# Kernel tuning notes

Measured on AMD Instinct MI355X. Metric: run time of the kernel, lower is better.

The kernel has to match this reference:

```python
import jax, jax.numpy as jnp
import numpy as np

B, Nq, C = 1, 40000, 256
Hh, L, P = 8, 4, 8
hd = C // Hh
LEVEL_SHAPES = [(128, 128), (64, 64), (32, 32), (16, 16)]


def setup_inputs() -> dict:
    key = jax.random.key(0)
    ks = jax.random.split(key, 16)
    inp = {}
    inp['query'] = jax.random.normal(ks[0], (B, Nq, C), jnp.float32)
    # reference points in [-1, 1] normalized coords (x, y)
    inp['reference_points'] = jax.random.uniform(ks[1], (B, Nq, L, 2), jnp.float32) * 2.0 - 1.0
    for i, (h, w) in enumerate(LEVEL_SHAPES):
        inp[f'feat{i}'] = jax.random.normal(ks[2 + i], (B, C, h, w), jnp.float32)
    # learned params (torch Linear y = x @ W + b, W stored as [in, out])
    inp['W_off'] = jax.random.normal(ks[6], (C, Hh * L * P * 2), jnp.float32) * 0.02
    inp['b_off'] = jax.random.normal(ks[7], (Hh * L * P * 2,), jnp.float32) * 0.5
    inp['W_attn'] = jax.random.normal(ks[8], (C, Hh * L * P), jnp.float32) * 0.02
    inp['b_attn'] = jnp.zeros((Hh * L * P,), jnp.float32)
    inp['W_val'] = jax.random.normal(ks[9], (C, C), jnp.float32) * (1.0 / np.sqrt(C))
    inp['b_val'] = jnp.zeros((C,), jnp.float32)
    inp['W_out'] = jax.random.normal(ks[10], (C, C), jnp.float32) * (1.0 / np.sqrt(C))
    inp['b_out'] = jnp.zeros((C,), jnp.float32)
    return inp


def _deform_sample(v, coords):
    # Bilinear grid_sample, align_corners=True, zeros padding.
    # v: [B, Hh, H, W, hd]; coords: [B, Hh, S, 2] in [-1, 1] (x, y)
    _, _, H, W, _ = v.shape
    x = (coords[..., 0] + 1.0) * 0.5 * (W - 1)
    y = (coords[..., 1] + 1.0) * 0.5 * (H - 1)
    x0 = jnp.floor(x)
    y0 = jnp.floor(y)
    vflat = v.reshape(v.shape[0], v.shape[1], H * W, v.shape[4])

    def corner(xi, yi, w):
        inb = (xi >= 0) & (xi <= W - 1) & (yi >= 0) & (yi <= H - 1)
        idx = (jnp.clip(yi, 0, H - 1) * W + jnp.clip(xi, 0, W - 1)).astype(jnp.int32)
        g = jnp.take_along_axis(vflat, idx[..., None], axis=2)  # [B,Hh,S,hd]
        return g * (w * inb)[..., None]

    return (corner(x0, y0, (x0 + 1 - x) * (y0 + 1 - y))
            + corner(x0 + 1, y0, (x - x0) * (y0 + 1 - y))
            + corner(x0, y0 + 1, (x0 + 1 - x) * (y - y0))
            + corner(x0 + 1, y0 + 1, (x - x0) * (y - y0)))


def reference(query, feat0, feat1, feat2, feat3, reference_points,
              W_off, b_off, W_attn, b_attn, W_val, b_val, W_out, b_out):
    feats = [feat0, feat1, feat2, feat3]
    off = (query @ W_off + b_off).reshape(B, Nq, Hh, L, P, 2)
    w = (query @ W_attn + b_attn).reshape(B, Nq, Hh, L, P)
    w = jax.nn.softmax(w, axis=-1)  # softmax over points, per level
    # samp: [B, Nq, Hh, L, P, 2]
    samp = reference_points[:, :, None, :, None, :] + jnp.tanh(off) * 0.25

    out = jnp.zeros((B, Nq, Hh, hd), jnp.float32)
    for l, f in enumerate(feats):
        Hl, Wl = f.shape[2], f.shape[3]
        v = jnp.einsum('bchw,cd->bhwd', f, W_val) + b_val  # value proj
        v = v.reshape(B, Hl, Wl, Hh, hd).transpose(0, 3, 1, 2, 4)  # [B,Hh,H,W,hd]
        coords = samp[:, :, :, l].transpose(0, 2, 1, 3, 4).reshape(B, Hh, Nq * P, 2)
        s = _deform_sample(v, coords).reshape(B, Hh, Nq, P, hd)
        wl = w[:, :, :, l].transpose(0, 2, 1, 3)  # [B,Hh,Nq,P]
        out = out + jnp.einsum('bhnpd,bhnp->bnhd', s, wl)

    return out.reshape(B, Nq, C) @ W_out + b_out
```

## Files before the change

### kernel.cpp

```cpp
#include <hip/hip_runtime.h>
#include <hip/hip_fp16.h>
#include <math.h>

#define NQ 40000

typedef short s16x8 __attribute__((ext_vector_type(8)));
typedef float f32x4 __attribute__((ext_vector_type(4)));

static constexpr int HLa[4] = {128, 64, 32, 16};
static constexpr int HWa[4] = {16384, 4096, 1024, 256};
static constexpr int VB[4] = {0, 4194304, 5242880, 5505024};

__device__ __forceinline__ short bf16hi(float x) {
    union { float f; unsigned u; } v; v.f = x;
    unsigned r = v.u + 0x7FFFu + ((v.u >> 16) & 1u);
    return (short)(r >> 16);
}
__device__ __forceinline__ float bf16f(short s) {
    union { unsigned u; float f; } v; v.u = ((unsigned)(unsigned short)s) << 16;
    return v.f;
}
__device__ __forceinline__ float fast_tanh(float x) {
    float xc = fminf(fmaxf(x, -15.f), 15.f);
    float e = __expf(2.f * xc);
    return (e - 1.f) / (e + 1.f);
}
#define MFMA16(a, b, c) __builtin_amdgcn_mfma_f32_16x16x32_bf16(a, b, c, 0, 0, 0)

__global__ __launch_bounds__(256) void prep_w(
    const float* __restrict__ Woff, const float* __restrict__ Wattn,
    const float* __restrict__ Wout, short* __restrict__ WtH, short* __restrict__ WtL)
{
    int r = blockIdx.x, c = threadIdx.x;
    float x;
    if (r < 512)      x = Woff[c * 512 + r];
    else if (r < 768) x = Wattn[c * 256 + (r - 512)];
    else              x = Wout[c * 256 + (r - 768)];
    short hi = bf16hi(x);
    WtH[r * 256 + c] = hi;
    WtL[r * 256 + c] = bf16hi(x - bf16f(hi));
}

__global__ __launch_bounds__(256) void vproj_kernel(
    const float* __restrict__ f0, const float* __restrict__ f1,
    const float* __restrict__ f2, const float* __restrict__ f3,
    const float* __restrict__ Wv, const float* __restrict__ bv,
    __half* __restrict__ v)
{
    __shared__ float fT[256 * 16];

    int bid = blockIdx.x;
    const float* f;
    int base, HWl, hw0;
    if (bid < 1024)      { f = f0; base = VB[0]; HWl = 16384; hw0 = bid * 16; }
    else if (bid < 1280) { f = f1; base = VB[1]; HWl = 4096;  hw0 = (bid - 1024) * 16; }
    else if (bid < 1344) { f = f2; base = VB[2]; HWl = 1024;  hw0 = (bid - 1280) * 16; }
    else                 { f = f3; base = VB[3]; HWl = 256;   hw0 = (bid - 1344) * 16; }

    int t = threadIdx.x;
    for (int k = 0; k < 16; ++k) {
        int idx = k * 256 + t;
        int c = idx >> 4, j = idx & 15;
        fT[idx] = f[c * HWl + hw0 + j];
    }
    __syncthreads();

    int to4 = (t & 63) * 4;
    int hw4 = (t >> 6) * 4;

    float4 bv4 = *(const float4*)(bv + to4);
    float acc[4][4];
    #pragma unroll
    for (int i = 0; i < 4; ++i) {
        acc[i][0] = bv4.x; acc[i][1] = bv4.y; acc[i][2] = bv4.z; acc[i][3] = bv4.w;
    }

    #pragma unroll 4
    for (int c = 0; c < 256; ++c) {
        float4 w4 = *(const float4*)(Wv + c * 256 + to4);
        float4 fv = *(const float4*)(fT + c * 16 + hw4);
        float fa[4] = {fv.x, fv.y, fv.z, fv.w};
        float wa[4] = {w4.x, w4.y, w4.z, w4.w};
        #pragma unroll
        for (int i = 0; i < 4; ++i)
            #pragma unroll
            for (int j = 0; j < 4; ++j)
                acc[i][j] += fa[i] * wa[j];
    }

    int hh = to4 >> 5, dd4 = to4 & 31;
    #pragma unroll
    for (int i = 0; i < 4; ++i) {
        int hw = hw0 + hw4 + i;
        __half2 h0 = __floats2half2_rn(acc[i][0], acc[i][1]);
        __half2 h1 = __floats2half2_rn(acc[i][2], acc[i][3]);
        uint2 st = make_uint2(*(unsigned*)&h0, *(unsigned*)&h1);
        *(uint2*)(v + base + (hh * HWl + hw) * 32 + dd4) = st;
    }
}

__global__ __launch_bounds__(256, 4) void msda_kernel(
    const float* __restrict__ query, const float* __restrict__ refp,
    const float* __restrict__ boff,  const float* __restrict__ battn,
    const float* __restrict__ bout,
    const short* __restrict__ WtH,   const short* __restrict__ WtL,
    const __half* __restrict__ v,    float* __restrict__ out)
{
    __shared__ __align__(16) char lds[28928];
    short*    sQh  = (short*)lds;
    short*    sQl  = (short*)(lds + 8448);
    __half*   sWh  = (__half*)(lds + 16896);
    float*    sR   = (float*)(lds + 28416);

    const int t = threadIdx.x;
    const int n0 = blockIdx.x * 16;
    const int wv = t >> 6, lane = t & 63;
    const int mrow = lane & 15, kg = lane >> 4;
    float*    offW = (float*)lds + wv * 1056;
    unsigned* sPIw = (unsigned*)(lds + 25344 + wv * 768);
    uint2*    sPWw = (uint2*)(lds + 25344 + wv * 768 + 256);
    __half*   preT = sWh;

    for (int k2 = 0; k2 < 16; ++k2) {
        float x = query[(n0 + k2) * 256 + t];
        short hi = bf16hi(x);
        sQh[k2 * 264 + t] = hi;
        sQl[k2 * 264 + t] = bf16hi(x - bf16f(hi));
    }
    if (t < 128) sR[t] = refp[n0 * 8 + t];
    __syncthreads();

    f32x4 accO[8], accA[4];
    {
        f32x4 z = {0.f, 0.f, 0.f, 0.f};
        #pragma unroll
        for (int j = 0; j < 8; ++j) accO[j] = z;
        #pragma unroll
        for (int j = 0; j < 4; ++j) accA[j] = z;
    }
    {
        const short* offH = WtH + (wv * 128 + mrow) * 256 + kg * 8;
        const short* offLo = WtL + (wv * 128 + mrow) * 256 + kg * 8;
        const short* attH = WtH + (512 + wv * 64 + mrow) * 256 + kg * 8;
        const short* attL = WtL + (512 + wv * 64 + mrow) * 256 + kg * 8;
        const int aoff = mrow * 264 + kg * 8;
        #pragma unroll
        for (int kk = 0; kk < 8; ++kk) {
            s16x8 ah = *(const s16x8*)(sQh + aoff + kk * 32);
            s16x8 al = *(const s16x8*)(sQl + aoff + kk * 32);
            #pragma unroll
            for (int j = 0; j < 8; ++j) {
                s16x8 bh = *(const s16x8*)(offH + j * 4096 + kk * 32);
                s16x8 bl = *(const s16x8*)(offLo + j * 4096 + kk * 32);
                accO[j] = MFMA16(ah, bh, accO[j]);
                accO[j] = MFMA16(al, bh, accO[j]);
                accO[j] = MFMA16(ah, bl, accO[j]);
            }
            #pragma unroll
            for (int ja = 0; ja < 4; ++ja) {
                s16x8 bh = *(const s16x8*)(attH + ja * 4096 + kk * 32);
                s16x8 bl = *(const s16x8*)(attL + ja * 4096 + kk * 32);
                accA[ja] = MFMA16(ah, bh, accA[ja]);
                accA[ja] = MFMA16(al, bh, accA[ja]);
                accA[ja] = MFMA16(ah, bl, accA[ja]);
            }
        }
    }
    #pragma unroll
    for (int j = 0; j < 8; ++j) {
        float bb = boff[wv * 128 + j * 16 + mrow];
        #pragma unroll
        for (int r = 0; r < 4; ++r) accO[j][r] += bb;
    }
    #pragma unroll
    for (int ja = 0; ja < 4; ++ja) {
        float bb = battn[wv * 64 + ja * 16 + mrow];
        #pragma unroll
        for (int r = 0; r < 4; ++r) accA[ja][r] += bb;
    }

    #pragma unroll
    for (int ja = 0; ja < 4; ++ja) {
        int hh = 2 * wv + (ja >> 1);
        int l  = ((ja & 1) << 1) | (mrow >> 3);
        int p  = mrow & 7;
        #pragma unroll
        for (int r = 0; r < 4; ++r) {
            float x = accA[ja][r];
            float m = fmaxf(x, __shfl_xor(x, 1));
            m = fmaxf(m, __shfl_xor(m, 2));
            m = fmaxf(m, __shfl_xor(m, 4));
            float e = __expf(x - m);
            float s = e + __shfl_xor(e, 1);
            s += __shfl_xor(s, 2);
            s += __shfl_xor(s, 4);
            int q = kg * 4 + r;
            sWh[q * 264 + hh * 32 + l * 8 + p] = __float2half_rn(e / s);
        }
    }
    __syncthreads();

    const int l_p = (lane >> 3) & 3, p_p = lane & 7, hhL_p = lane >> 5;
    const int Wl_p = 128 >> l_p;
    const float scl_p = 0.5f * (float)(Wl_p - 1);
    const int whCol = (2 * wv + hhL_p) * 32 + l_p * 8 + p_p;
    const int sg = kg, ch2 = mrow;
    const int Wl_s = 128 >> sg;
    const int HWs = Wl_s * Wl_s;
    const int dyoMul = Wl_s * 16;
    const int VBs = (sg == 0) ? VB[0] : (sg == 1) ? VB[1] : (sg == 2) ? VB[2] : VB[3];
    const __half2* vl0 = (const __half2*)(v + VBs + (2 * wv) * HWs * 32) + ch2;
    const __half2* vl1 = (const __half2*)(v + VBs + (2 * wv + 1) * HWs * 32) + ch2;

    for (int sp = 0; sp < 2; ++sp) {
        if ((kg >> 1) == sp) {
            #pragma unroll
            for (int j = 0; j < 8; ++j)
                #pragma unroll
                for (int r = 0; r < 4; ++r)
                    offW[((kg & 1) * 4 + r) * 132 + j * 16 + mrow] = accO[j][r];
        }

        for (int c8 = 0; c8 < 8; ++c8) {
            const int chunk = sp * 8 + c8;
            {
                float2 ll = *(const float2*)(offW + c8 * 132 + 2 * lane);
                float lx = ll.x, ly = ll.y;
                float w  = __half2float(sWh[chunk * 264 + whCol]);
                float rx = sR[chunk * 8 + l_p * 2], ry = sR[chunk * 8 + l_p * 2 + 1];
                float cx = rx + fast_tanh(lx) * 0.25f;
                float cy = ry + fast_tanh(ly) * 0.25f;
                float xx = (cx + 1.f) * scl_p, yy = (cy + 1.f) * scl_p;
                float x0f = floorf(xx), y0f = floorf(yy);
                float fx = xx - x0f, fy = yy - y0f;
                int x0 = (int)x0f, y0 = (int)y0f;
                int xc0 = min(max(x0, 0), Wl_p - 1);
                int xc1 = min(max(x0 + 1, 0), Wl_p - 1);
                int yc0 = min(max(y0, 0), Wl_p - 1);
                int yc1 = min(max(y0 + 1, 0), Wl_p - 1);
                bool bx0 = (x0 >= 0) & (x0 < Wl_p);
                bool bx1 = (x0 + 1 >= 0) & (x0 + 1 < Wl_p);
                bool by0 = (y0 >= 0) & (y0 < Wl_p);
                bool by1 = (y0 + 1 >= 0) & (y0 + 1 < Wl_p);
                float w00 = (bx0 && by0) ? (1.f - fx) * (1.f - fy) * w : 0.f;
                float w01 = (bx1 && by0) ? fx * (1.f - fy) * w : 0.f;
                float w10 = (bx0 && by1) ? (1.f - fx) * fy * w : 0.f;
                float w11 = (bx1 && by1) ? fx * fy * w : 0.f;
                unsigned pw = (unsigned)(yc0 * Wl_p + xc0)
                            | ((unsigned)(xc1 - xc0) << 14)
                            | ((unsigned)(yc1 - yc0) << 15);
                sPIw[lane] = pw;
                __half2 hA = __floats2half2_rn(w00, w01);
                __half2 hB = __floats2half2_rn(w10, w11);
                sPWw[lane] = make_uint2(*(unsigned*)&hA, *(unsigned*)&hB);
            }

            float ax = 0.f, ay = 0.f;
            #pragma unroll
            for (int iter = 0; iter < 16; ++iter) {
                const int hhL = iter >> 3, p = iter & 7;
                const int rec = hhL * 32 + sg * 8 + p;
                unsigned pw = sPIw[rec];
                uint2 ww = sPWw[rec];
                const __half2* vl = hhL ? vl1 : vl0;
                int idx = pw & 0x3FFF;
                int dxo = ((pw >> 14) & 1) * 16;
                int dyo = ((pw >> 15) & 1) * dyoMul;
                const __half2* b00 = vl + idx * 16;
                float2 fa = __half22float2(*(__half2*)&ww.x);
                float2 fb = __half22float2(*(__half2*)&ww.y);
                float2 f00 = __half22float2(b00[0]);
                float2 f01 = __half22float2(b00[dxo]);
                float2 f10 = __half22float2(b00[dyo]);
                float2 f11 = __half22float2(b00[dxo + dyo]);
                ax += fa.x * f00.x + fa.y * f01.x + fb.x * f10.x + fb.y * f11.x;
                ay += fa.x * f00.y + fa.y * f01.y + fb.x * f10.y + fb.y * f11.y;
                if ((iter & 7) == 7) {
                    float sxv = ax + __shfl_xor(ax, 16); sxv += __shfl_xor(sxv, 32);
                    float syv = ay + __shfl_xor(ay, 16); syv += __shfl_xor(syv, 32);
                    if (sg == 0)
                        *(__half2*)(preT + chunk * 264 + (2 * wv + hhL) * 32 + ch2 * 2) =
                            __floats2half2_rn(sxv, syv);
                    ax = 0.f; ay = 0.f;
                }
            }
        }
    }
    __syncthreads();

    {
        int q = t & 15, seg = t >> 4;
        const __half2* src = (const __half2*)(preT + q * 264 + seg * 16);
        short* dh = sQh + q * 264 + seg * 16;
        short* dl = sQl + q * 264 + seg * 16;
        #pragma unroll
        for (int jj = 0; jj < 8; ++jj) {
            float2 f = __half22float2(src[jj]);
            short h0 = bf16hi(f.x), h1 = bf16hi(f.y);
            dh[2 * jj]     = h0;
            dh[2 * jj + 1] = h1;
            dl[2 * jj]     = bf16hi(f.x - bf16f(h0));
            dl[2 * jj + 1] = bf16hi(f.y - bf16f(h1));
        }
    }
    __syncthreads();

    {
        f32x4 accE[4];
        f32x4 z = {0.f, 0.f, 0.f, 0.f};
        #pragma unroll
        for (int e = 0; e < 4; ++e) accE[e] = z;
        const short* outH = WtH + (768 + wv * 64 + mrow) * 256 + kg * 8;
        const short* outL = WtL + (768 + wv * 64 + mrow) * 256 + kg * 8;
        const int aoff = mrow * 264 + kg * 8;
        #pragma unroll
        for (int kk = 0; kk < 8; ++kk) {
            s16x8 ah = *(const s16x8*)(sQh + aoff + kk * 32);
            s16x8 al = *(const s16x8*)(sQl + aoff + kk * 32);
            #pragma unroll
            for (int e = 0; e < 4; ++e) {
                s16x8 bh = *(const s16x8*)(outH + e * 4096 + kk * 32);
                s16x8 bl = *(const s16x8*)(outL + e * 4096 + kk * 32);
                accE[e] = MFMA16(ah, bh, accE[e]);
                accE[e] = MFMA16(al, bh, accE[e]);
                accE[e] = MFMA16(ah, bl, accE[e]);
            }
        }
        #pragma unroll
        for (int e = 0; e < 4; ++e) {
            int col = wv * 64 + e * 16 + mrow;
            float bb = bout[col];
            #pragma unroll
            for (int r = 0; r < 4; ++r)
                out[(n0 + kg * 4 + r) * 256 + col] = accE[e][r] + bb;
        }
    }
}

extern "C" void kernel_launch(void* const* d_in, const int* in_sizes, int n_in,
                              void* d_out, int out_size, void* d_ws, size_t ws_size,
                              hipStream_t stream) {
    const float* query = (const float*)d_in[0];
    const float* refp  = (const float*)d_in[1];
    const float* f0    = (const float*)d_in[2];
    const float* f1    = (const float*)d_in[3];
    const float* f2    = (const float*)d_in[4];
    const float* f3    = (const float*)d_in[5];
    const float* Woff  = (const float*)d_in[6];
    const float* boff  = (const float*)d_in[7];
    const float* Wattn = (const float*)d_in[8];
    const float* battn = (const float*)d_in[9];
    const float* Wval  = (const float*)d_in[10];
    const float* bval  = (const float*)d_in[11];
    const float* Wout  = (const float*)d_in[12];
    const float* bout  = (const float*)d_in[13];

    __half* v  = (__half*)d_ws;
    short* WtH = (short*)((char*)d_ws + 11141120);
    short* WtL = WtH + 262144;
    float* outp = (float*)d_out;

    prep_w<<<1024, 256, 0, stream>>>(Woff, Wattn, Wout, WtH, WtL);
    vproj_kernel<<<1360, 256, 0, stream>>>(f0, f1, f2, f3, Wval, bval, v);
    msda_kernel<<<2500, 256, 0, stream>>>(query, refp, boff, battn, bout,
                                          WtH, WtL, v, outp);
}
```

Before: 498.7 us.

## Double-buffer sampling records and overlap next-chunk packing with gathers

Splits the per-wave sampling-record buffers into two LDS slots and computes the next chunk's coordinates and bilinear weights while the current chunk's value gathers are in flight. The gather loop is also restructured to issue all four corner loads for four points before consuming them, which exposes more memory-level parallelism. The cost is more LDS per block and higher register pressure from the batched loads, which could reduce occupancy under the 256x4 launch bound.

```diff
diff --git a/kernel.cpp b/kernel.cpp
--- a/kernel.cpp
+++ b/kernel.cpp
@@ -99,6 +99,38 @@
     }
 }
 
+#define PACK_REC(CHUNK, DPI, DPW) do {                                        \
+    float2 ll = *(const float2*)(offW + ((CHUNK) & 7) * 132 + 2 * lane);      \
+    float lx = ll.x, ly = ll.y;                                               \
+    float w  = __half2float(sWh[(CHUNK) * 264 + whCol]);                      \
+    float rx = sR[(CHUNK) * 8 + l_p * 2], ry = sR[(CHUNK) * 8 + l_p * 2 + 1]; \
+    float cx = rx + fast_tanh(lx) * 0.25f;                                    \
+    float cy = ry + fast_tanh(ly) * 0.25f;                                    \
+    float xx = (cx + 1.f) * scl_p, yy = (cy + 1.f) * scl_p;                   \
+    float x0f = floorf(xx), y0f = floorf(yy);                                 \
+    float fx = xx - x0f, fy = yy - y0f;                                       \
+    int x0 = (int)x0f, y0 = (int)y0f;                                         \
+    int xc0 = min(max(x0, 0), Wl_p - 1);                                      \
+    int xc1 = min(max(x0 + 1, 0), Wl_p - 1);                                  \
+    int yc0 = min(max(y0, 0), Wl_p - 1);                                      \
+    int yc1 = min(max(y0 + 1, 0), Wl_p - 1);                                  \
+    bool bx0 = (x0 >= 0) & (x0 < Wl_p);                                       \
+    bool bx1 = (x0 + 1 >= 0) & (x0 + 1 < Wl_p);                               \
+    bool by0 = (y0 >= 0) & (y0 < Wl_p);                                       \
+    bool by1 = (y0 + 1 >= 0) & (y0 + 1 < Wl_p);                               \
+    float w00 = (bx0 && by0) ? (1.f - fx) * (1.f - fy) * w : 0.f;             \
+    float w01 = (bx1 && by0) ? fx * (1.f - fy) * w : 0.f;                     \
+    float w10 = (bx0 && by1) ? (1.f - fx) * fy * w : 0.f;                     \
+    float w11 = (bx1 && by1) ? fx * fy * w : 0.f;                             \
+    unsigned pw = (unsigned)(yc0 * Wl_p + xc0)                                \
+                | ((unsigned)(xc1 - xc0) << 14)                               \
+                | ((unsigned)(yc1 - yc0) << 15);                              \
+    (DPI)[lane] = pw;                                                         \
+    __half2 hA = __floats2half2_rn(w00, w01);                                 \
+    __half2 hB = __floats2half2_rn(w10, w11);                                 \
+    (DPW)[lane] = make_uint2(*(unsigned*)&hA, *(unsigned*)&hB);               \
+} while (0)
+
 __global__ __launch_bounds__(256, 4) void msda_kernel(
     const float* __restrict__ query, const float* __restrict__ refp,
     const float* __restrict__ boff,  const float* __restrict__ battn,
@@ -106,19 +138,21 @@
     const short* __restrict__ WtH,   const short* __restrict__ WtL,
     const __half* __restrict__ v,    float* __restrict__ out)
 {
-    __shared__ __align__(16) char lds[28928];
+    __shared__ __align__(16) char lds[32000];
     short*    sQh  = (short*)lds;
     short*    sQl  = (short*)(lds + 8448);
     __half*   sWh  = (__half*)(lds + 16896);
-    float*    sR   = (float*)(lds + 28416);
+    float*    sR   = (float*)(lds + 31488);
 
     const int t = threadIdx.x;
     const int n0 = blockIdx.x * 16;
     const int wv = t >> 6, lane = t & 63;
     const int mrow = lane & 15, kg = lane >> 4;
     float*    offW = (float*)lds + wv * 1056;
-    unsigned* sPIw = (unsigned*)(lds + 25344 + wv * 768);
-    uint2*    sPWw = (uint2*)(lds + 25344 + wv * 768 + 256);
+    unsigned* sPI0 = (unsigned*)(lds + 25344 + wv * 768);
+    uint2*    sPW0 = (uint2*)(lds + 25344 + wv * 768 + 256);
+    unsigned* sPI1 = (unsigned*)(lds + 28416 + wv * 768);
+    uint2*    sPW1 = (uint2*)(lds + 28416 + wv * 768 + 256);
     __half*   preT = sWh;
 
     for (int k2 = 0; k2 < 16; ++k2) {
@@ -204,6 +238,7 @@
     const int Wl_p = 128 >> l_p;
     const float scl_p = 0.5f * (float)(Wl_p - 1);
     const int whCol = (2 * wv + hhL_p) * 32 + l_p * 8 + p_p;
+    (void)p_p;
     const int sg = kg, ch2 = mrow;
     const int Wl_s = 128 >> sg;
     const int HWs = Wl_s * Wl_s;
@@ -220,69 +255,61 @@
                 for (int r = 0; r < 4; ++r)
                     offW[((kg & 1) * 4 + r) * 132 + j * 16 + mrow] = accO[j][r];
         }
-
+        PACK_REC(sp * 8, sPI0, sPW0);
+
+        #pragma unroll 2
         for (int c8 = 0; c8 < 8; ++c8) {
             const int chunk = sp * 8 + c8;
-            {
-                float2 ll = *(const float2*)(offW + c8 * 132 + 2 * lane);
-                float lx = ll.x, ly = ll.y;
-                float w  = __half2float(sWh[chunk * 264 + whCol]);
-                float rx = sR[chunk * 8 + l_p * 2], ry = sR[chunk * 8 + l_p * 2 + 1];
-                float cx = rx + fast_tanh(lx) * 0.25f;
-                float cy = ry + fast_tanh(ly) * 0.25f;
-                float xx = (cx + 1.f) * scl_p, yy = (cy + 1.f) * scl_p;
-                float x0f = floorf(xx), y0f = floorf(yy);
-                float fx = xx - x0f, fy = yy - y0f;
-                int x0 = (int)x0f, y0 = (int)y0f;
-                int xc0 = min(max(x0, 0), Wl_p - 1);
-                int xc1 = min(max(x0 + 1, 0), Wl_p - 1);
-                int yc0 = min(max(y0, 0), Wl_p - 1);
-                int yc1 = min(max(y0 + 1, 0), Wl_p - 1);
-                bool bx0 = (x0 >= 0) & (x0 < Wl_p);
-                bool bx1 = (x0 + 1 >= 0) & (x0 + 1 < Wl_p);
-                bool by0 = (y0 >= 0) & (y0 < Wl_p);
-                bool by1 = (y0 + 1 >= 0) & (y0 + 1 < Wl_p);
-                float w00 = (bx0 && by0) ? (1.f - fx) * (1.f - fy) * w : 0.f;
-                float w01 = (bx1 && by0) ? fx * (1.f - fy) * w : 0.f;
-                float w10 = (bx0 && by1) ? (1.f - fx) * fy * w : 0.f;
-                float w11 = (bx1 && by1) ? fx * fy * w : 0.f;
-                unsigned pw = (unsigned)(yc0 * Wl_p + xc0)
-                            | ((unsigned)(xc1 - xc0) << 14)
-                            | ((unsigned)(yc1 - yc0) << 15);
-                sPIw[lane] = pw;
-                __half2 hA = __floats2half2_rn(w00, w01);
-                __half2 hB = __floats2half2_rn(w10, w11);
-                sPWw[lane] = make_uint2(*(unsigned*)&hA, *(unsigned*)&hB);
-            }
-
-            float ax = 0.f, ay = 0.f;
-            #pragma unroll
-            for (int iter = 0; iter < 16; ++iter) {
-                const int hhL = iter >> 3, p = iter & 7;
-                const int rec = hhL * 32 + sg * 8 + p;
-                unsigned pw = sPIw[rec];
-                uint2 ww = sPWw[rec];
+            unsigned* sPIc = (c8 & 1) ? sPI1 : sPI0;
+            uint2*    sPWc = (c8 & 1) ? sPW1 : sPW0;
+            unsigned* nPI  = (c8 & 1) ? sPI0 : sPI1;
+            uint2*    nPW  = (c8 & 1) ? sPW0 : sPW1;
+
+            #pragma unroll
+            for (int hhL = 0; hhL < 2; ++hhL) {
                 const __half2* vl = hhL ? vl1 : vl0;
-                int idx = pw & 0x3FFF;
-                int dxo = ((pw >> 14) & 1) * 16;
-                int dyo = ((pw >> 15) & 1) * dyoMul;
-                const __half2* b00 = vl + idx * 16;
-                float2 fa = __half22float2(*(__half2*)&ww.x);
-                float2 fb = __half22float2(*(__half2*)&ww.y);
-                float2 f00 = __half22float2(b00[0]);
-                float2 f01 = __half22float2(b00[dxo]);
-                float2 f10 = __half22float2(b00[dyo]);
-                float2 f11 = __half22float2(b00[dxo + dyo]);
-                ax += fa.x * f00.x + fa.y * f01.x + fb.x * f10.x + fb.y * f11.x;
-                ay += fa.x * f00.y + fa.y * f01.y + fb.x * f10.y + fb.y * f11.y;
-                if ((iter & 7) == 7) {
-                    float sxv = ax + __shfl_xor(ax, 16); sxv += __shfl_xor(sxv, 32);
-                    float syv = ay + __shfl_xor(ay, 16); syv += __shfl_xor(syv, 32);
-                    if (sg == 0)
-                        *(__half2*)(preT + chunk * 264 + (2 * wv + hhL) * 32 + ch2 * 2) =
-                            __floats2half2_rn(sxv, syv);
-                    ax = 0.f; ay = 0.f;
+                float ax = 0.f, ay = 0.f;
+                #pragma unroll
+                for (int pg = 0; pg < 2; ++pg) {
+                    unsigned pwv[4]; uint2 wwv[4];
+                    unsigned q00[4], q01[4], q10[4], q11[4];
+                    #pragma unroll
+                    for (int p4 = 0; p4 < 4; ++p4) {
+                        int rec = hhL * 32 + sg * 8 + pg * 4 + p4;
+                        pwv[p4] = sPIc[rec];
+                        wwv[p4] = sPWc[rec];
+                    }
+                    #pragma unroll
+                    for (int p4 = 0; p4 < 4; ++p4) {
+                        int idx = pwv[p4] & 0x3FFF;
+                        int dxo = ((pwv[p4] >> 14) & 1) * 16;
+                        int dyo = ((pwv[p4] >> 15) & 1) * dyoMul;
+                        const __half2* b00 = vl + idx * 16;
+                        q00[p4] = *(const unsigned*)b00;
+                        q01[p4] = *(const unsigned*)(b00 + dxo);
+                        q10[p4] = *(const unsigned*)(b00 + dyo);
+                        q11[p4] = *(const unsigned*)(b00 + dxo + dyo);
+                    }
+                    if (hhL == 0 && pg == 0 && c8 < 7) {
+                        PACK_REC(chunk + 1, nPI, nPW);
+                    }
+                    #pragma unroll
+                    for (int p4 = 0; p4 < 4; ++p4) {
+                        float2 fa = __half22float2(*(__half2*)&wwv[p4].x);
+                        float2 fb = __half22float2(*(__half2*)&wwv[p4].y);
+                        float2 f00 = __half22float2(*(__half2*)&q00[p4]);
+                        float2 f01 = __half22float2(*(__half2*)&q01[p4]);
+                        float2 f10 = __half22float2(*(__half2*)&q10[p4]);
+                        float2 f11 = __half22float2(*(__half2*)&q11[p4]);
+                        ax += fa.x * f00.x + fa.y * f01.x + fb.x * f10.x + fb.y * f11.x;
+                        ay += fa.x * f00.y + fa.y * f01.y + fb.x * f10.y + fb.y * f11.y;
+                    }
                 }
+                float sxv = ax + __shfl_xor(ax, 16); sxv += __shfl_xor(sxv, 32);
+                float syv = ay + __shfl_xor(ay, 16); syv += __shfl_xor(syv, 32);
+                if (sg == 0)
+                    *(__half2*)(preT + chunk * 264 + (2 * wv + hhL) * 32 + ch2 * 2) =
+                        __floats2half2_rn(sxv, syv);
             }
         }
     }
```

Result: no change. 498.3 us (-0.1%).

## Split fused deformable attention into logits, gather and output-projection kernels

Applied to the files above, without the earlier changes.

Breaks the single fused MSDA kernel into three kernels. The first computes offset/attention logits and packs the sampling indices and weights into global buffers, the second is a dedicated high-occupancy bilinear gather, and the third is the output projection. The aim is to decouple the latency-bound gather from the MFMA-heavy projections so each runs with suitable occupancy. The cost is large global intermediate buffers and extra kernel launches, and the fused path is kept as a fallback when the workspace is too small.

```diff
diff --git a/kernel.cpp b/kernel.cpp
--- a/kernel.cpp
+++ b/kernel.cpp
@@ -99,7 +99,248 @@
     }
 }
 
-__global__ __launch_bounds__(256, 4) void msda_kernel(
+__global__ __launch_bounds__(256, 4) void logits_pack_kernel(
+    const float* __restrict__ query, const float* __restrict__ refp,
+    const float* __restrict__ boff,  const float* __restrict__ battn,
+    const short* __restrict__ WtH,   const short* __restrict__ WtL,
+    unsigned* __restrict__ PIg,      uint2* __restrict__ PWg)
+{
+    __shared__ __align__(16) char lds[42752];
+    short*  sQh = (short*)lds;
+    short*  sQl = (short*)(lds + 8448);
+    __half* sWh = (__half*)(lds + 33792);
+    float*  sR  = (float*)(lds + 42240);
+
+    const int t = threadIdx.x;
+    const int n0 = blockIdx.x * 16;
+    const int wv = t >> 6, lane = t & 63;
+    const int mrow = lane & 15, kg = lane >> 4;
+    float* offW = (float*)lds + wv * 2112;
+
+    for (int k2 = 0; k2 < 16; ++k2) {
+        float x = query[(n0 + k2) * 256 + t];
+        short hi = bf16hi(x);
+        sQh[k2 * 264 + t] = hi;
+        sQl[k2 * 264 + t] = bf16hi(x - bf16f(hi));
+    }
+    if (t < 128) sR[t] = refp[n0 * 8 + t];
+    __syncthreads();
+
+    f32x4 accO[8], accA[4];
+    {
+        f32x4 z = {0.f, 0.f, 0.f, 0.f};
+        #pragma unroll
+        for (int j = 0; j < 8; ++j) accO[j] = z;
+        #pragma unroll
+        for (int j = 0; j < 4; ++j) accA[j] = z;
+    }
+    {
+        const short* offH = WtH + (wv * 128 + mrow) * 256 + kg * 8;
+        const short* offLo = WtL + (wv * 128 + mrow) * 256 + kg * 8;
+        const short* attH = WtH + (512 + wv * 64 + mrow) * 256 + kg * 8;
+        const short* attL = WtL + (512 + wv * 64 + mrow) * 256 + kg * 8;
+        const int aoff = mrow * 264 + kg * 8;
+        #pragma unroll
+        for (int kk = 0; kk < 8; ++kk) {
+            s16x8 ah = *(const s16x8*)(sQh + aoff + kk * 32);
+            s16x8 al = *(const s16x8*)(sQl + aoff + kk * 32);
+            #pragma unroll
+            for (int j = 0; j < 8; ++j) {
+                s16x8 bh = *(const s16x8*)(offH + j * 4096 + kk * 32);
+                s16x8 bl = *(const s16x8*)(offLo + j * 4096 + kk * 32);
+                accO[j] = MFMA16(ah, bh, accO[j]);
+                accO[j] = MFMA16(al, bh, accO[j]);
+                accO[j] = MFMA16(ah, bl, accO[j]);
+            }
+            #pragma unroll
+            for (int ja = 0; ja < 4; ++ja) {
+                s16x8 bh = *(const s16x8*)(attH + ja * 4096 + kk * 32);
+                s16x8 bl = *(const s16x8*)(attL + ja * 4096 + kk * 32);
+                accA[ja] = MFMA16(ah, bh, accA[ja]);
+                accA[ja] = MFMA16(al, bh, accA[ja]);
+                accA[ja] = MFMA16(ah, bl, accA[ja]);
+            }
+        }
+    }
+    #pragma unroll
+    for (int j = 0; j < 8; ++j) {
+        float bb = boff[wv * 128 + j * 16 + mrow];
+        #pragma unroll
+        for (int r = 0; r < 4; ++r) accO[j][r] += bb;
+    }
+    #pragma unroll
+    for (int ja = 0; ja < 4; ++ja) {
+        float bb = battn[wv * 64 + ja * 16 + mrow];
+        #pragma unroll
+        for (int r = 0; r < 4; ++r) accA[ja][r] += bb;
+    }
+    __syncthreads();
+
+    #pragma unroll
+    for (int j = 0; j < 8; ++j)
+        #pragma unroll
+        for (int r = 0; r < 4; ++r)
+            offW[(kg * 4 + r) * 132 + j * 16 + mrow] = accO[j][r];
+
+    #pragma unroll
+    for (int ja = 0; ja < 4; ++ja) {
+        int hh = 2 * wv + (ja >> 1);
+        int l  = ((ja & 1) << 1) | (mrow >> 3);
+        int p  = mrow & 7;
+        #pragma unroll
+        for (int r = 0; r < 4; ++r) {
+            float x = accA[ja][r];
+            float m = fmaxf(x, __shfl_xor(x, 1));
+            m = fmaxf(m, __shfl_xor(m, 2));
+            m = fmaxf(m, __shfl_xor(m, 4));
+            float e = __expf(x - m);
+            float s = e + __shfl_xor(e, 1);
+            s += __shfl_xor(s, 2);
+            s += __shfl_xor(s, 4);
+            int q = kg * 4 + r;
+            sWh[q * 264 + hh * 32 + l * 8 + p] = __float2half_rn(e / s);
+        }
+    }
+
+    const int l_p = (lane >> 3) & 3, p_p = lane & 7, hhL_p = lane >> 5;
+    (void)p_p; (void)hhL_p;
+    const int Wl_p = 128 >> l_p;
+    const float scl_p = 0.5f * (float)(Wl_p - 1);
+    const int whCol = (2 * wv + (lane >> 5)) * 32 + l_p * 8 + (lane & 7);
+
+    for (int chunk = 0; chunk < 16; ++chunk) {
+        float2 ll = *(const float2*)(offW + chunk * 132 + 2 * lane);
+        float lx = ll.x, ly = ll.y;
+        float w  = __half2float(sWh[chunk * 264 + whCol]);
+        float rx = sR[chunk * 8 + l_p * 2], ry = sR[chunk * 8 + l_p * 2 + 1];
+        float cx = rx + fast_tanh(lx) * 0.25f;
+        float cy = ry + fast_tanh(ly) * 0.25f;
+        float xx = (cx + 1.f) * scl_p, yy = (cy + 1.f) * scl_p;
+        float x0f = floorf(xx), y0f = floorf(yy);
+        float fx = xx - x0f, fy = yy - y0f;
+        int x0 = (int)x0f, y0 = (int)y0f;
+        int xc0 = min(max(x0, 0), Wl_p - 1);
+        int xc1 = min(max(x0 + 1, 0), Wl_p - 1);
+        int yc0 = min(max(y0, 0), Wl_p - 1);
+        int yc1 = min(max(y0 + 1, 0), Wl_p - 1);
+        bool bx0 = (x0 >= 0) & (x0 < Wl_p);
+        bool bx1 = (x0 + 1 >= 0) & (x0 + 1 < Wl_p);
+        bool by0 = (y0 >= 0) & (y0 < Wl_p);
+        bool by1 = (y0 + 1 >= 0) & (y0 + 1 < Wl_p);
+        float w00 = (bx0 && by0) ? (1.f - fx) * (1.f - fy) * w : 0.f;
+        float w01 = (bx1 && by0) ? fx * (1.f - fy) * w : 0.f;
+        float w10 = (bx0 && by1) ? (1.f - fx) * fy * w : 0.f;
+        float w11 = (bx1 && by1) ? fx * fy * w : 0.f;
+        unsigned pw = (unsigned)(yc0 * Wl_p + xc0)
+                    | ((unsigned)(xc1 - xc0) << 14)
+                    | ((unsigned)(yc1 - yc0) << 15);
+        __half2 hA = __floats2half2_rn(w00, w01);
+        __half2 hB = __floats2half2_rn(w10, w11);
+        int gi = (n0 + chunk) * 256 + wv * 64 + lane;
+        PIg[gi] = pw;
+        PWg[gi] = make_uint2(*(unsigned*)&hA, *(unsigned*)&hB);
+    }
+}
+
+__global__ __launch_bounds__(256, 6) void gather_kernel(
+    const unsigned* __restrict__ PIg, const uint2* __restrict__ PWg,
+    const __half* __restrict__ v,     __half* __restrict__ preTg)
+{
+    int tid = blockIdx.x * 256 + threadIdx.x;
+    int q   = tid >> 7;
+    int hh  = (tid >> 4) & 7;
+    int ch2 = tid & 15;
+    const unsigned* PIq = PIg + q * 256 + hh * 32;
+    const uint2*    PWq = PWg + q * 256 + hh * 32;
+
+    float ax = 0.f, ay = 0.f;
+    #pragma unroll
+    for (int l = 0; l < 4; ++l) {
+        const __half2* vl = (const __half2*)(v + VB[l] + hh * HWa[l] * 32) + ch2;
+        const int dyoMul = HLa[l] * 16;
+        #pragma unroll
+        for (int p = 0; p < 8; ++p) {
+            unsigned pw = PIq[l * 8 + p];
+            uint2 ww = PWq[l * 8 + p];
+            int idx = pw & 0x3FFF;
+            int dxo = ((pw >> 14) & 1) * 16;
+            int dyo = ((pw >> 15) & 1) * dyoMul;
+            const __half2* b00 = vl + idx * 16;
+            float2 fa = __half22float2(*(__half2*)&ww.x);
+            float2 fb = __half22float2(*(__half2*)&ww.y);
+            float2 f00 = __half22float2(b00[0]);
+            float2 f01 = __half22float2(b00[dxo]);
+            float2 f10 = __half22float2(b00[dyo]);
+            float2 f11 = __half22float2(b00[dxo + dyo]);
+            ax += fa.x * f00.x + fa.y * f01.x + fb.x * f10.x + fb.y * f11.x;
+            ay += fa.x * f00.y + fa.y * f01.y + fb.x * f10.y + fb.y * f11.y;
+        }
+    }
+    ((__half2*)preTg)[tid] = __floats2half2_rn(ax, ay);
+}
+
+__global__ __launch_bounds__(256, 4) void outproj_kernel(
+    const __half* __restrict__ preTg, const short* __restrict__ WtH,
+    const short* __restrict__ WtL,    const float* __restrict__ bout,
+    float* __restrict__ out)
+{
+    __shared__ __align__(16) char lds[16896];
+    short* sQh = (short*)lds;
+    short* sQl = (short*)(lds + 8448);
+
+    const int t = threadIdx.x;
+    const int n0 = blockIdx.x * 16;
+    const int wv = t >> 6, lane = t & 63;
+    const int mrow = lane & 15, kg = lane >> 4;
+
+    {
+        int q = t & 15, seg = t >> 4;
+        const __half2* src = (const __half2*)(preTg + (n0 + q) * 256 + seg * 16);
+        short* dh = sQh + q * 264 + seg * 16;
+        short* dl = sQl + q * 264 + seg * 16;
+        #pragma unroll
+        for (int jj = 0; jj < 8; ++jj) {
+            float2 f = __half22float2(src[jj]);
+            short h0 = bf16hi(f.x), h1 = bf16hi(f.y);
+            dh[2 * jj]     = h0;
+            dh[2 * jj + 1] = h1;
+            dl[2 * jj]     = bf16hi(f.x - bf16f(h0));
+            dl[2 * jj + 1] = bf16hi(f.y - bf16f(h1));
+        }
+    }
+    __syncthreads();
+
+    f32x4 accE[4];
+    f32x4 z = {0.f, 0.f, 0.f, 0.f};
+    #pragma unroll
+    for (int e = 0; e < 4; ++e) accE[e] = z;
+    const short* outH = WtH + (768 + wv * 64 + mrow) * 256 + kg * 8;
+    const short* outL = WtL + (768 + wv * 64 + mrow) * 256 + kg * 8;
+    const int aoff = mrow * 264 + kg * 8;
+    #pragma unroll
+    for (int kk = 0; kk < 8; ++kk) {
+        s16x8 ah = *(const s16x8*)(sQh + aoff + kk * 32);
+        s16x8 al = *(const s16x8*)(sQl + aoff + kk * 32);
+        #pragma unroll
+        for (int e = 0; e < 4; ++e) {
+            s16x8 bh = *(const s16x8*)(outH + e * 4096 + kk * 32);
+            s16x8 bl = *(const s16x8*)(outL + e * 4096 + kk * 32);
+            accE[e] = MFMA16(ah, bh, accE[e]);
+            accE[e] = MFMA16(al, bh, accE[e]);
+            accE[e] = MFMA16(ah, bl, accE[e]);
+        }
+    }
+    #pragma unroll
+    for (int e = 0; e < 4; ++e) {
+        int col = wv * 64 + e * 16 + mrow;
+        float bb = bout[col];
+        #pragma unroll
+        for (int r = 0; r < 4; ++r)
+            out[(n0 + kg * 4 + r) * 256 + col] = accE[e][r] + bb;
+    }
+}
+
+__global__ __launch_bounds__(256, 4) void msda_fused(
     const float* __restrict__ query, const float* __restrict__ refp,
     const float* __restrict__ boff,  const float* __restrict__ battn,
     const float* __restrict__ bout,
@@ -220,7 +461,6 @@
                 for (int r = 0; r < 4; ++r)
                     offW[((kg & 1) * 4 + r) * 132 + j * 16 + mrow] = accO[j][r];
         }
-
         for (int c8 = 0; c8 < 8; ++c8) {
             const int chunk = sp * 8 + c8;
             {
@@ -254,7 +494,6 @@
                 __half2 hB = __floats2half2_rn(w10, w11);
                 sPWw[lane] = make_uint2(*(unsigned*)&hA, *(unsigned*)&hB);
             }
-
             float ax = 0.f, ay = 0.f;
             #pragma unroll
             for (int iter = 0; iter < 16; ++iter) {
@@ -355,13 +594,25 @@
     const float* Wout  = (const float*)d_in[12];
     const float* bout  = (const float*)d_in[13];
 
-    __half* v  = (__half*)d_ws;
-    short* WtH = (short*)((char*)d_ws + 11141120);
-    short* WtL = WtH + 262144;
+    char* ws = (char*)d_ws;
+    __half* v  = (__half*)ws;
+    short* WtH = (short*)(ws + 11141120);
+    short* WtL = (short*)(ws + 11665408);
+    unsigned* PIg = (unsigned*)(ws + 12189696);
+    uint2*    PWg = (uint2*)(ws + 53149696);
+    __half*   preTg = (__half*)(ws + 135069696);
     float* outp = (float*)d_out;
 
     prep_w<<<1024, 256, 0, stream>>>(Woff, Wattn, Wout, WtH, WtL);
     vproj_kernel<<<1360, 256, 0, stream>>>(f0, f1, f2, f3, Wval, bval, v);
-    msda_kernel<<<2500, 256, 0, stream>>>(query, refp, boff, battn, bout,
-                                          WtH, WtL, v, outp);
-}
+
+    if (ws_size >= (size_t)155549696) {
+        logits_pack_kernel<<<2500, 256, 0, stream>>>(query, refp, boff, battn,
+                                                     WtH, WtL, PIg, PWg);
+        gather_kernel<<<20000, 256, 0, stream>>>(PIg, PWg, v, preTg);
+        outproj_kernel<<<2500, 256, 0, stream>>>(preTg, WtH, WtL, bout, outp);
+    } else {
+        msda_fused<<<2500, 256, 0, stream>>>(query, refp, boff, battn, bout,
+                                             WtH, WtL, v, outp);
+    }
+}
```

After: 610.0 us. +22.3%, slower.

## Split MSDA kernel by head-pair with separate output projection kernel

Applied to the files above, without the earlier changes.

Each block now handles 64 queries for one pair of heads, selected by blockIdx&3, instead of 16 queries across all heads. Sampling for a given head pair touches only that pair's slice of the value tensor, which should improve cache locality. The output projection moves into its own kernel that reads an fp16 intermediate from global workspace. The cost is an extra launch and a global round trip of the intermediate, and query is re-read by the 4 head-pair blocks, with bf16 hi/lo splitting done in registers.

```diff
diff --git a/kernel.cpp b/kernel.cpp
--- a/kernel.cpp
+++ b/kernel.cpp
@@ -99,35 +99,27 @@
     }
 }
 
-__global__ __launch_bounds__(256, 4) void msda_kernel(
+__global__ __launch_bounds__(256, 4) void msda_hp_kernel(
     const float* __restrict__ query, const float* __restrict__ refp,
     const float* __restrict__ boff,  const float* __restrict__ battn,
-    const float* __restrict__ bout,
     const short* __restrict__ WtH,   const short* __restrict__ WtL,
-    const __half* __restrict__ v,    float* __restrict__ out)
+    const __half* __restrict__ v,    __half* __restrict__ preTg)
 {
-    __shared__ __align__(16) char lds[28928];
-    short*    sQh  = (short*)lds;
-    short*    sQl  = (short*)(lds + 8448);
-    __half*   sWh  = (__half*)(lds + 16896);
-    float*    sR   = (float*)(lds + 28416);
+    __shared__ __align__(16) char lds[30720];
+    __half* sWh = (__half*)(lds + 16896);
+    float*  sR  = (float*)(lds + 28672);
 
     const int t = threadIdx.x;
-    const int n0 = blockIdx.x * 16;
+    const int hp = blockIdx.x & 3;
+    const int n0 = (blockIdx.x >> 2) * 64;
     const int wv = t >> 6, lane = t & 63;
     const int mrow = lane & 15, kg = lane >> 4;
     float*    offW = (float*)lds + wv * 1056;
-    unsigned* sPIw = (unsigned*)(lds + 25344 + wv * 768);
-    uint2*    sPWw = (uint2*)(lds + 25344 + wv * 768 + 256);
-    __half*   preT = sWh;
-
-    for (int k2 = 0; k2 < 16; ++k2) {
-        float x = query[(n0 + k2) * 256 + t];
-        short hi = bf16hi(x);
-        sQh[k2 * 264 + t] = hi;
-        sQl[k2 * 264 + t] = bf16hi(x - bf16f(hi));
-    }
-    if (t < 128) sR[t] = refp[n0 * 8 + t];
+    unsigned* sPIw = (unsigned*)(lds + 25600 + wv * 768);
+    uint2*    sPWw = (uint2*)(lds + 25600 + wv * 768 + 256);
+
+    sR[t]       = refp[n0 * 8 + t];
+    sR[t + 256] = refp[n0 * 8 + t + 256];
     __syncthreads();
 
     f32x4 accO[8], accA[4];
@@ -139,15 +131,23 @@
         for (int j = 0; j < 4; ++j) accA[j] = z;
     }
     {
-        const short* offH = WtH + (wv * 128 + mrow) * 256 + kg * 8;
-        const short* offLo = WtL + (wv * 128 + mrow) * 256 + kg * 8;
-        const short* attH = WtH + (512 + wv * 64 + mrow) * 256 + kg * 8;
-        const short* attL = WtL + (512 + wv * 64 + mrow) * 256 + kg * 8;
-        const int aoff = mrow * 264 + kg * 8;
+        const float* qrow = query + (n0 + wv * 16 + mrow) * 256 + kg * 8;
+        const short* offH = WtH + (hp * 128 + mrow) * 256 + kg * 8;
+        const short* offLo = WtL + (hp * 128 + mrow) * 256 + kg * 8;
+        const short* attH = WtH + (512 + hp * 64 + mrow) * 256 + kg * 8;
+        const short* attL = WtL + (512 + hp * 64 + mrow) * 256 + kg * 8;
         #pragma unroll
         for (int kk = 0; kk < 8; ++kk) {
-            s16x8 ah = *(const s16x8*)(sQh + aoff + kk * 32);
-            s16x8 al = *(const s16x8*)(sQl + aoff + kk * 32);
+            float4 qa = *(const float4*)(qrow + kk * 32);
+            float4 qb = *(const float4*)(qrow + kk * 32 + 4);
+            float qv[8] = {qa.x, qa.y, qa.z, qa.w, qb.x, qb.y, qb.z, qb.w};
+            s16x8 ah, al;
+            #pragma unroll
+            for (int e = 0; e < 8; ++e) {
+                short hi = bf16hi(qv[e]);
+                ah[e] = hi;
+                al[e] = bf16hi(qv[e] - bf16f(hi));
+            }
             #pragma unroll
             for (int j = 0; j < 8; ++j) {
                 s16x8 bh = *(const s16x8*)(offH + j * 4096 + kk * 32);
@@ -168,22 +168,22 @@
     }
     #pragma unroll
     for (int j = 0; j < 8; ++j) {
-        float bb = boff[wv * 128 + j * 16 + mrow];
+        float bb = boff[hp * 128 + j * 16 + mrow];
         #pragma unroll
         for (int r = 0; r < 4; ++r) accO[j][r] += bb;
     }
     #pragma unroll
     for (int ja = 0; ja < 4; ++ja) {
-        float bb = battn[wv * 64 + ja * 16 + mrow];
+        float bb = battn[hp * 64 + ja * 16 + mrow];
         #pragma unroll
         for (int r = 0; r < 4; ++r) accA[ja][r] += bb;
     }
 
     #pragma unroll
     for (int ja = 0; ja < 4; ++ja) {
-        int hh = 2 * wv + (ja >> 1);
-        int l  = ((ja & 1) << 1) | (mrow >> 3);
-        int p  = mrow & 7;
+        int hhL = ja >> 1;
+        int l   = ((ja & 1) << 1) | (mrow >> 3);
+        int p   = mrow & 7;
         #pragma unroll
         for (int r = 0; r < 4; ++r) {
             float x = accA[ja][r];
@@ -194,23 +194,21 @@
             float s = e + __shfl_xor(e, 1);
             s += __shfl_xor(s, 2);
             s += __shfl_xor(s, 4);
-            int q = kg * 4 + r;
-            sWh[q * 264 + hh * 32 + l * 8 + p] = __float2half_rn(e / s);
-        }
-    }
-    __syncthreads();
-
-    const int l_p = (lane >> 3) & 3, p_p = lane & 7, hhL_p = lane >> 5;
+            int ql = wv * 16 + kg * 4 + r;
+            sWh[ql * 68 + hhL * 32 + l * 8 + p] = __float2half_rn(e / s);
+        }
+    }
+
+    const int l_p = (lane >> 3) & 3;
     const int Wl_p = 128 >> l_p;
     const float scl_p = 0.5f * (float)(Wl_p - 1);
-    const int whCol = (2 * wv + hhL_p) * 32 + l_p * 8 + p_p;
     const int sg = kg, ch2 = mrow;
     const int Wl_s = 128 >> sg;
     const int HWs = Wl_s * Wl_s;
     const int dyoMul = Wl_s * 16;
     const int VBs = (sg == 0) ? VB[0] : (sg == 1) ? VB[1] : (sg == 2) ? VB[2] : VB[3];
-    const __half2* vl0 = (const __half2*)(v + VBs + (2 * wv) * HWs * 32) + ch2;
-    const __half2* vl1 = (const __half2*)(v + VBs + (2 * wv + 1) * HWs * 32) + ch2;
+    const __half2* vl0 = (const __half2*)(v + VBs + (2 * hp) * HWs * 32) + ch2;
+    const __half2* vl1 = (const __half2*)(v + VBs + (2 * hp + 1) * HWs * 32) + ch2;
 
     for (int sp = 0; sp < 2; ++sp) {
         if ((kg >> 1) == sp) {
@@ -223,11 +221,12 @@
 
         for (int c8 = 0; c8 < 8; ++c8) {
             const int chunk = sp * 8 + c8;
+            const int ql = wv * 16 + chunk;
             {
                 float2 ll = *(const float2*)(offW + c8 * 132 + 2 * lane);
                 float lx = ll.x, ly = ll.y;
-                float w  = __half2float(sWh[chunk * 264 + whCol]);
-                float rx = sR[chunk * 8 + l_p * 2], ry = sR[chunk * 8 + l_p * 2 + 1];
+                float w  = __half2float(sWh[ql * 68 + lane]);
+                float rx = sR[ql * 8 + l_p * 2], ry = sR[ql * 8 + l_p * 2 + 1];
                 float cx = rx + fast_tanh(lx) * 0.25f;
                 float cy = ry + fast_tanh(ly) * 0.25f;
                 float xx = (cx + 1.f) * scl_p, yy = (cy + 1.f) * scl_p;
@@ -279,18 +278,32 @@
                     float sxv = ax + __shfl_xor(ax, 16); sxv += __shfl_xor(sxv, 32);
                     float syv = ay + __shfl_xor(ay, 16); syv += __shfl_xor(syv, 32);
                     if (sg == 0)
-                        *(__half2*)(preT + chunk * 264 + (2 * wv + hhL) * 32 + ch2 * 2) =
+                        *(__half2*)(preTg + (n0 + ql) * 256 + (2 * hp + hhL) * 32 + ch2 * 2) =
                             __floats2half2_rn(sxv, syv);
                     ax = 0.f; ay = 0.f;
                 }
             }
         }
     }
-    __syncthreads();
+}
+
+__global__ __launch_bounds__(256, 4) void outproj_kernel(
+    const __half* __restrict__ preTg, const short* __restrict__ WtH,
+    const short* __restrict__ WtL,    const float* __restrict__ bout,
+    float* __restrict__ out)
+{
+    __shared__ __align__(16) char lds[16896];
+    short* sQh = (short*)lds;
+    short* sQl = (short*)(lds + 8448);
+
+    const int t = threadIdx.x;
+    const int n0 = blockIdx.x * 16;
+    const int wv = t >> 6, lane = t & 63;
+    const int mrow = lane & 15, kg = lane >> 4;
 
     {
         int q = t & 15, seg = t >> 4;
-        const __half2* src = (const __half2*)(preT + q * 264 + seg * 16);
+        const __half2* src = (const __half2*)(preTg + (n0 + q) * 256 + seg * 16);
         short* dh = sQh + q * 264 + seg * 16;
         short* dl = sQl + q * 264 + seg * 16;
         #pragma unroll
@@ -305,35 +318,33 @@
     }
     __syncthreads();
 
-    {
-        f32x4 accE[4];
-        f32x4 z = {0.f, 0.f, 0.f, 0.f};
-        #pragma unroll
-        for (int e = 0; e < 4; ++e) accE[e] = z;
-        const short* outH = WtH + (768 + wv * 64 + mrow) * 256 + kg * 8;
-        const short* outL = WtL + (768 + wv * 64 + mrow) * 256 + kg * 8;
-        const int aoff = mrow * 264 + kg * 8;
-        #pragma unroll
-        for (int kk = 0; kk < 8; ++kk) {
-            s16x8 ah = *(const s16x8*)(sQh + aoff + kk * 32);
-            s16x8 al = *(const s16x8*)(sQl + aoff + kk * 32);
-            #pragma unroll
-            for (int e = 0; e < 4; ++e) {
-                s16x8 bh = *(const s16x8*)(outH + e * 4096 + kk * 32);
-                s16x8 bl = *(const s16x8*)(outL + e * 4096 + kk * 32);
-                accE[e] = MFMA16(ah, bh, accE[e]);
-                accE[e] = MFMA16(al, bh, accE[e]);
-                accE[e] = MFMA16(ah, bl, accE[e]);
-            }
-        }
+    f32x4 accE[4];
+    f32x4 z = {0.f, 0.f, 0.f, 0.f};
+    #pragma unroll
+    for (int e = 0; e < 4; ++e) accE[e] = z;
+    const short* outH = WtH + (768 + wv * 64 + mrow) * 256 + kg * 8;
+    const short* outL = WtL + (768 + wv * 64 + mrow) * 256 + kg * 8;
+    const int aoff = mrow * 264 + kg * 8;
+    #pragma unroll
+    for (int kk = 0; kk < 8; ++kk) {
+        s16x8 ah = *(const s16x8*)(sQh + aoff + kk * 32);
+        s16x8 al = *(const s16x8*)(sQl + aoff + kk * 32);
         #pragma unroll
         for (int e = 0; e < 4; ++e) {
-            int col = wv * 64 + e * 16 + mrow;
-            float bb = bout[col];
-            #pragma unroll
-            for (int r = 0; r < 4; ++r)
-                out[(n0 + kg * 4 + r) * 256 + col] = accE[e][r] + bb;
-        }
+            s16x8 bh = *(const s16x8*)(outH + e * 4096 + kk * 32);
+            s16x8 bl = *(const s16x8*)(outL + e * 4096 + kk * 32);
+            accE[e] = MFMA16(ah, bh, accE[e]);
+            accE[e] = MFMA16(al, bh, accE[e]);
+            accE[e] = MFMA16(ah, bl, accE[e]);
+        }
+    }
+    #pragma unroll
+    for (int e = 0; e < 4; ++e) {
+        int col = wv * 64 + e * 16 + mrow;
+        float bb = bout[col];
+        #pragma unroll
+        for (int r = 0; r < 4; ++r)
+            out[(n0 + kg * 4 + r) * 256 + col] = accE[e][r] + bb;
     }
 }
 
@@ -355,13 +366,16 @@
     const float* Wout  = (const float*)d_in[12];
     const float* bout  = (const float*)d_in[13];
 
-    __half* v  = (__half*)d_ws;
-    short* WtH = (short*)((char*)d_ws + 11141120);
-    short* WtL = WtH + 262144;
+    char* ws = (char*)d_ws;
+    __half* v  = (__half*)ws;
+    short* WtH = (short*)(ws + 11141120);
+    short* WtL = (short*)(ws + 11665408);
+    __half* preTg = (__half*)(ws + 12189696);
     float* outp = (float*)d_out;
 
     prep_w<<<1024, 256, 0, stream>>>(Woff, Wattn, Wout, WtH, WtL);
     vproj_kernel<<<1360, 256, 0, stream>>>(f0, f1, f2, f3, Wval, bval, v);
-    msda_kernel<<<2500, 256, 0, stream>>>(query, refp, boff, battn, bout,
-                                          WtH, WtL, v, outp);
-}
+    msda_hp_kernel<<<2500, 256, 0, stream>>>(query, refp, boff, battn,
+                                             WtH, WtL, v, preTg);
+    outproj_kernel<<<2500, 256, 0, stream>>>(preTg, WtH, WtL, bout, outp);
+}
```

Result: slower. 536.7 us (+7.6%).
